# Kernel tuning notes

Measured on AMD Instinct MI355X. Metric: run time of the kernel, lower is better.

Reference implementation:

```python
import jax, jax.numpy as jnp
import numpy as np

B, N, NG, K, H, C, BD = 4, 2048, 12, 16, 64, 128, 64
M = N // 4  # fps with down_sample=4
TWO_PI = 2.0 * np.pi


def _knn_idx(q, x, k):
    # q [Q,3] queries, x [P,3] pool -> [Q,k] indices of k nearest points in x
    d2 = jnp.sum((q[:, None, :] - x[None, :, :]) ** 2, axis=-1)
    _, idx = jax.lax.top_k(-d2, k)
    return idx


def _fps_idx(pos, m):
    # farthest point sampling, fixed m points, start at index 0
    n = pos.shape[0]
    def body(carry, _):
        d, last = carry
        dist = jnp.sum((pos - pos[last]) ** 2, axis=-1)
        d = jnp.minimum(d, dist)
        return (d, jnp.argmax(d)), last
    (_, _), idx = jax.lax.scan(body, (jnp.full((n,), 1e10, pos.dtype), jnp.int32(0)), None, length=m)
    return idx


def _basis_mlp(z, rff_w, w1, b1, w2, b2):
    # RFF -> Linear -> GELU -> Linear -> GELU
    p = TWO_PI * (z @ rff_w)
    f = jnp.concatenate([jnp.sin(p), jnp.cos(p)], axis=-1)
    h = jax.nn.gelu(f @ w1 + b1)
    return jax.nn.gelu(h @ w2 + b2)


def _interaction(x, nbr, kbx, kbR, kx_w, kx_b, kR_w, kR_b, mix_w, mix_b):
    # depthwise separable group conv: spatial gather-multiply-mean, then orientation mix
    kx = kbx @ kx_w + kx_b                     # [M,K,NG,C] spatial depthwise kernel
    kR = kbR @ kR_w + kR_b                     # [NG,NG,C] orientation depthwise kernel
    agg = jnp.mean(x[nbr] * kx, axis=1)        # [M,NG,C] mean over K neighbors
    y = jnp.einsum('bnc,mnc->bmc', agg, kR) / kR.shape[0]
    return x + jax.nn.gelu(y @ mix_w + mix_b)


def setup_inputs():
    key = jax.random.key(0)
    ks = iter(jax.random.split(key, 64))
    def randn(shape, std=1.0):
        return std * jax.random.normal(next(ks), shape, dtype=jnp.float32)
    inp = {}
    inp['pos'] = jax.random.uniform(next(ks), (B, N, 3), dtype=jnp.float32)
    nrm = randn((B, N, 3))
    inp['normal'] = nrm / jnp.linalg.norm(nrm, axis=-1, keepdims=True)
    g = randn((NG, 3))
    inp['grid'] = g / jnp.linalg.norm(g, axis=-1, keepdims=True)
    def lin(name, fin, fout):
        inp[name + '_w'] = randn((fin, fout), 1.0 / np.sqrt(fin))
        inp[name + '_b'] = jnp.zeros((fout,), jnp.float32)
    lin('emb1', 4, H); lin('emb2', H, H)
    lin('down', H, C)
    inp['bx_rff'] = randn((2, C // 2), 10.0)   # sigma=10
    lin('bx1', C, C); lin('bx2', C, BD)
    inp['bR_rff'] = randn((1, C // 2), 10.0)
    lin('bR1', C, C); lin('bR2', C, BD)
    for j in ('i1', 'i2'):
        lin(j + '_kx', BD, C); lin(j + '_kR', BD, C); lin(j + '_mix', C, C)
    lin('post1', C, 256); lin('post2', 256, 64); lin('post3', 64, 1)
    return inp


def reference(pos, normal, grid, emb1_w, emb1_b, emb2_w, emb2_b, down_w, down_b,
              bx_rff, bx1_w, bx1_b, bx2_w, bx2_b, bR_rff, bR1_w, bR1_b, bR2_w, bR2_b,
              i1_kx_w, i1_kx_b, i1_kR_w, i1_kR_b, i1_mix_w, i1_mix_b,
              i2_kx_w, i2_kx_b, i2_kR_w, i2_kR_b, i2_mix_w, i2_mix_b,
              post1_w, post1_b, post2_w, post2_b, post3_w, post3_b):
    def per_graph(p, nm):
        # lift: fiber features = <grid, normal> plus broadcast positions -> [N,NG,4]
        feat = jnp.concatenate([(nm @ grid.T)[:, :, None],
                                jnp.broadcast_to(p[:, None, :], (p.shape[0], NG, 3))], axis=-1)
        x = jax.nn.gelu(feat @ emb1_w + emb1_b) @ emb2_w + emb2_b   # [N,NG,H]
        # downsample block: fps + knn + linear/relu + scatter-max (exactly K edges per target)
        sel = _fps_idx(p, M)
        nbr_d = _knn_idx(p[sel], p, K)                               # [M,K] into N
        h = jax.nn.relu(x @ down_w + down_b)                         # [N,NG,C]
        x = jnp.max(h[nbr_d], axis=1)                                # [M,NG,C]
        ps = p[sel]
        # convolver block: knn graph + r3s2 edge attrs + basis MLPs + 2 interaction layers
        nbr = _knn_idx(ps, ps, K)                                    # [M,K] into M
        rel = ps[nbr] - ps[:, None, :]                               # pos[src]-pos[tgt], [M,K,3]
        rz = jnp.einsum('mke,ne->mkn', rel, grid)                    # [M,K,NG]
        rxy = jnp.sqrt(jnp.sum((rel[:, :, None, :] - rz[..., None] * grid) ** 2, axis=-1) + 1e-12)
        rpx = jnp.stack([rxy, rz], axis=-1)                          # [M,K,NG,2]
        rpR = (grid @ grid.T)[:, :, None]                            # [NG,NG,1]
        kbx = _basis_mlp(rpx, bx_rff, bx1_w, bx1_b, bx2_w, bx2_b)    # [M,K,NG,BD]
        kbR = _basis_mlp(rpR, bR_rff, bR1_w, bR1_b, bR2_w, bR2_b)    # [NG,NG,BD]
        x = _interaction(x, nbr, kbx, kbR, i1_kx_w, i1_kx_b, i1_kR_w, i1_kR_b, i1_mix_w, i1_mix_b)
        x = _interaction(x, nbr, kbx, kbR, i2_kx_w, i2_kx_b, i2_kR_w, i2_kR_b, i2_mix_w, i2_mix_b)
        # readout: mean over grid, global mean pool, MLP head
        g = jnp.mean(x, axis=(0, 1))                                 # [C]
        h1 = jax.nn.gelu(g @ post1_w + post1_b)
        h2 = jax.nn.gelu(h1 @ post2_w + post2_b)
        return h2 @ post3_w + post3_b                                # [1]
    return jax.vmap(per_graph)(pos, normal)                          # [B,1]
```

## Files before the change

### kernel.cpp

```cpp
#include <hip/hip_runtime.h>
#include <hip/hip_bf16.h>
#include <cfloat>

#define B_ 4
#define N_ 2048
#define NG_ 12
#define K_ 16
#define H_ 64
#define C_ 128
#define BD_ 64
#define M_ 512

typedef __attribute__((ext_vector_type(8))) short short8;
typedef __attribute__((ext_vector_type(4))) float floatx4;
typedef unsigned short ushort_t;
typedef unsigned int uint_t;

__device__ __forceinline__ float gelu_f(float x){
  float s = 0.7978845608028654f*(x + 0.044715f*x*x*x);
  float e = __expf(2.0f*s);
  float t = 1.0f - 2.0f/(e + 1.0f);
  return 0.5f*x*(1.0f + t);
}

__device__ __forceinline__ ushort_t bf16_rne(float x){
  uint_t u = __float_as_uint(x);
  uint_t r = (u + 0x7fffu + ((u >> 16) & 1u)) >> 16;
  return (ushort_t)r;
}

__device__ __forceinline__ uint_t pack_hl(float x){
  ushort_t hi = bf16_rne(x);
  float hif = __uint_as_float(((uint_t)hi)<<16);
  ushort_t lo = bf16_rne(x - hif);
  return (uint_t)hi | ((uint_t)lo << 16);
}

__device__ __forceinline__ uint_t cvtpk_bf16(float a, float b){
  uint_t r;
  asm("v_cvt_pk_bf16_f32 %0, %1, %2" : "=v"(r) : "v"(a), "v"(b));
  return r;
}

__device__ __forceinline__ void split2(float v0, float v1, uint_t& hp, uint_t& lp){
  hp = cvtpk_bf16(v0, v1);
  float h0 = __uint_as_float(hp << 16);
  float h1 = __uint_as_float(hp & 0xffff0000u);
  lp = cvtpk_bf16(v0 - h0, v1 - h1);
}

__device__ __forceinline__ uint_t pack_hl2(float v){
  uint_t hp = cvtpk_bf16(v, v);
  float hf = __uint_as_float(hp << 16);
  uint_t lp = cvtpk_bf16(v - hf, v - hf);
  return (hp & 0xffffu) | (lp << 16);
}

__device__ __forceinline__ uint_t perm_lo16(uint_t a, uint_t b){ return __builtin_amdgcn_perm(a, b, 0x05040100u); }
__device__ __forceinline__ uint_t perm_hi16(uint_t a, uint_t b){ return __builtin_amdgcn_perm(a, b, 0x07060302u); }

#define UNPACK8(Q0, Q1, AH, AL) { \
  uint_t* _ap = (uint_t*)&(AH); uint_t* _lp = (uint_t*)&(AL); \
  _ap[0] = perm_lo16((Q0).y, (Q0).x); _ap[1] = perm_lo16((Q0).w, (Q0).z); \
  _ap[2] = perm_lo16((Q1).y, (Q1).x); _ap[3] = perm_lo16((Q1).w, (Q1).z); \
  _lp[0] = perm_hi16((Q0).y, (Q0).x); _lp[1] = perm_hi16((Q0).w, (Q0).z); \
  _lp[2] = perm_hi16((Q1).y, (Q1).x); _lp[3] = perm_hi16((Q1).w, (Q1).z); }

#define DPP_AMAX(CTRL) { \
  int _vb = __float_as_int(v); \
  int _ov = __builtin_amdgcn_update_dpp(_vb, _vb, (CTRL), 0xF, 0xF, false); \
  int _oi = __builtin_amdgcn_update_dpp(vi, vi, (CTRL), 0xF, 0xF, false); \
  float _of = __int_as_float(_ov); \
  bool _tk = (_of > v) || (_of == v && _oi < vi); \
  v = _tk ? _of : v; vi = _tk ? _oi : vi; }

#define DPP_AMIN(CTRL) { \
  int _vb = __float_as_int(v); \
  int _ov = __builtin_amdgcn_update_dpp(_vb, _vb, (CTRL), 0xF, 0xF, false); \
  int _oi = __builtin_amdgcn_update_dpp(vi, vi, (CTRL), 0xF, 0xF, false); \
  float _of = __int_as_float(_ov); \
  bool _tk = (_of < v) || (_of == v && _oi < vi); \
  v = _tk ? _of : v; vi = _tk ? _oi : vi; }

#define FPSB 4
#define LIFTB (B_*N_*NG_/4)
#define WSB 64
#define KBRB (NG_*NG_)
#define PM4B 32

__global__ __launch_bounds__(256) void k_mega1(
    const float* __restrict__ pos, const float* __restrict__ normal,
    const float* __restrict__ grid,
    const float* __restrict__ e1w, const float* __restrict__ e1b,
    const float* __restrict__ e2w, const float* __restrict__ e2b,
    uint_t* __restrict__ x1p, float* __restrict__ ps,
    float4* __restrict__ pos4, float4* __restrict__ ps4,
    const float* __restrict__ bx1w, const float* __restrict__ bx2w,
    const float* __restrict__ kxw1, const float* __restrict__ kxw2,
    const float* __restrict__ dww,
    ushort_t* __restrict__ w1hiT, ushort_t* __restrict__ w1loT,
    ushort_t* __restrict__ w2hiT, ushort_t* __restrict__ w2loT,
    ushort_t* __restrict__ x1hiT, ushort_t* __restrict__ x1loT,
    ushort_t* __restrict__ x2hiT, ushort_t* __restrict__ x2loT,
    ushort_t* __restrict__ dwThi, ushort_t* __restrict__ dwTlo,
    const float* __restrict__ bR_rff,
    const float* __restrict__ bR1w, const float* __restrict__ bR1b,
    const float* __restrict__ bR2w, const float* __restrict__ bR2b,
    const float* __restrict__ kR1w, const float* __restrict__ kR1b,
    const float* __restrict__ kR2w, const float* __restrict__ kR2b,
    float* __restrict__ kRb1, float* __restrict__ kRb2){
  __shared__ float4 posS4[N_];
  __shared__ float2 wred[2][4];
  __shared__ int sidxS[M_];
  __shared__ float ts4[4][64];
  __shared__ float fsb[128], hsb[128];
  int bid = blockIdx.x;
  int tid = threadIdx.x;

  if (bid < FPSB){
    int b = bid;
    for (int i=tid;i<N_;i+=256){
      const float* p = pos + (size_t)b*N_*3 + (size_t)i*3;
      posS4[i] = make_float4(p[0], p[1], p[2], 0.f);
    }
    __syncthreads();
    float px[8],py[8],pz[8],d[8];
    #pragma unroll
    for (int j=0;j<8;++j){
      float4 pt = posS4[tid + 256*j];
      px[j]=pt.x; py[j]=pt.y; pz[j]=pt.z;
      d[j]=1e10f;
    }
    int wave = tid>>6, lane = tid&63;
    int last = 0;
    for (int s=0;s<M_;++s){
      if (tid==0) sidxS[s] = last;
      if (s==M_-1) break;
      float4 lp = posS4[last];
      float lx=lp.x, ly=lp.y, lz=lp.z;
      #pragma unroll
      for (int j=0;j<8;++j){
        float dx=__fsub_rn(px[j],lx), dy=__fsub_rn(py[j],ly), dz=__fsub_rn(pz[j],lz);
        float dist=__fadd_rn(__fadd_rn(__fmul_rn(dx,dx),__fmul_rn(dy,dy)),__fmul_rn(dz,dz));
        d[j]=fminf(d[j],dist);
      }
      float va = d[1]>d[0]?d[1]:d[0]; int ja = d[1]>d[0]?1:0;
      float vb = d[3]>d[2]?d[3]:d[2]; int jb = d[3]>d[2]?3:2;
      float vc = d[5]>d[4]?d[5]:d[4]; int jc = d[5]>d[4]?5:4;
      float vd = d[7]>d[6]?d[7]:d[6]; int jd = d[7]>d[6]?7:6;
      float ve = vb>va?vb:va; int je = vb>va?jb:ja;
      float vf = vd>vc?vd:vc; int jf = vd>vc?jd:jc;
      float v  = vf>ve?vf:ve; int jj = vf>ve?jf:je;
      int vi = tid + (jj<<8);
      DPP_AMAX(0x121); DPP_AMAX(0x122); DPP_AMAX(0x124); DPP_AMAX(0x128);
      DPP_AMAX(0x142); DPP_AMAX(0x143);
      int sv = __builtin_amdgcn_readlane(__float_as_int(v), 63);
      int si = __builtin_amdgcn_readlane(vi, 63);
      if (lane==0) wred[s&1][wave] = make_float2(__int_as_float(sv), __int_as_float(si));
      __syncthreads();
      float2 r0 = wred[s&1][0], r1 = wred[s&1][1], r2 = wred[s&1][2], r3 = wred[s&1][3];
      float bv = r0.x; int bi = __float_as_int(r0.y);
      int i1 = __float_as_int(r1.y); if (r1.x>bv || (r1.x==bv && i1<bi)){ bv=r1.x; bi=i1; }
      int i2 = __float_as_int(r2.y); if (r2.x>bv || (r2.x==bv && i2<bi)){ bv=r2.x; bi=i2; }
      int i3 = __float_as_int(r3.y); if (r3.x>bv || (r3.x==bv && i3<bi)){ bv=r3.x; bi=i3; }
      last = bi;
    }
    __syncthreads();
    for (int i=tid; i<M_; i+=256){
      float4 p = posS4[sidxS[i]];
      float* o = ps + ((size_t)b*M_+i)*3;
      o[0]=p.x; o[1]=p.y; o[2]=p.z;
      ps4[(size_t)b*M_+i] = make_float4(p.x, p.y, p.z, 0.f);
    }
  } else if (bid < FPSB + LIFTB){
    int vbid = bid - FPSB;
    int q = tid>>6, lane = tid&63;
    int fid = vbid*4 + q;
    int g = fid % NG_;
    int n = (fid / NG_) % N_;
    int b = fid / (NG_*N_);
    const float* nm = normal + (size_t)(b*N_+n)*3;
    const float* pp = pos + (size_t)(b*N_+n)*3;
    const float* gg = grid + g*3;
    float f0 = nm[0]*gg[0] + nm[1]*gg[1] + nm[2]*gg[2];
    float t = e1b[lane] + f0*e1w[lane] + pp[0]*e1w[64+lane] + pp[1]*e1w[128+lane] + pp[2]*e1w[192+lane];
    ts4[q][lane] = gelu_f(t);
    __syncthreads();
    float acc = e2b[lane];
    #pragma unroll
    for (int i=0;i<64;++i) acc = fmaf(ts4[q][i], e2w[i*64+lane], acc);
    x1p[(size_t)fid*64 + lane] = pack_hl(acc);
  } else if (bid < FPSB + LIFTB + WSB){
    int tg = (bid - FPSB - LIFTB)*256 + tid;
    if (tg < 16384){
      int j = tg >> 7, k = tg & 127;
      float x = bx1w[k*128 + j];
      ushort_t hi = bf16_rne(x);
      float hif = __uint_as_float(((uint_t)hi)<<16);
      ushort_t lo = bf16_rne(x - hif);
      w1hiT[tg] = hi; w1loT[tg] = lo;
    }
    if (tg < 8192){
      int c = tg >> 7, j = tg & 127;
      float x = bx2w[j*64 + c];
      ushort_t hi = bf16_rne(x);
      float hif = __uint_as_float(((uint_t)hi)<<16);
      ushort_t lo = bf16_rne(x - hif);
      w2hiT[tg] = hi; w2loT[tg] = lo;
    }
    if (tg < 8192){
      int c = tg >> 6, d = tg & 63;
      float xa = kxw1[d*128 + c];
      ushort_t hi = bf16_rne(xa);
      float hif = __uint_as_float(((uint_t)hi)<<16);
      ushort_t lo = bf16_rne(xa - hif);
      x1hiT[tg] = hi; x1loT[tg] = lo;
      float xb = kxw2[d*128 + c];
      ushort_t hi2 = bf16_rne(xb);
      float hif2 = __uint_as_float(((uint_t)hi2)<<16);
      ushort_t lo2 = bf16_rne(xb - hif2);
      x2hiT[tg] = hi2; x2loT[tg] = lo2;
      float xd = dww[d*128 + c];
      ushort_t hi3 = bf16_rne(xd);
      float hif3 = __uint_as_float(((uint_t)hi3)<<16);
      ushort_t lo3 = bf16_rne(xd - hif3);
      dwThi[tg] = hi3; dwTlo[tg] = lo3;
    }
  } else if (bid < FPSB + LIFTB + WSB + KBRB){
    int vbid = bid - FPSB - LIFTB - WSB;
    int gm = vbid / NG_, gn = vbid % NG_;
    int j = tid;
    if (j < 128){
      float z = grid[gm*3]*grid[gn*3] + grid[gm*3+1]*grid[gn*3+1] + grid[gm*3+2]*grid[gn*3+2];
      float ang = 6.283185307179586f * (z * bR_rff[j & 63]);
      fsb[j] = (j<64) ? sinf(ang) : cosf(ang);
    }
    __syncthreads();
    if (j < 128){
      float acc = bR1b[j];
      for (int i=0;i<128;++i) acc = fmaf(fsb[i], bR1w[i*128+j], acc);
      hsb[j] = gelu_f(acc);
    }
    __syncthreads();
    if (j < 64){
      float a2 = bR2b[j];
      for (int i=0;i<128;++i) a2 = fmaf(hsb[i], bR2w[i*64+j], a2);
      fsb[j] = gelu_f(a2);
    }
    __syncthreads();
    if (j < 128){
      float a1 = kR1b[j], a2v = kR2b[j];
      for (int d=0; d<64; ++d){
        float kv = fsb[d];
        a1  = fmaf(kv, kR1w[d*128+j], a1);
        a2v = fmaf(kv, kR2w[d*128+j], a2v);
      }
      kRb1[(size_t)vbid*128 + j] = a1;
      kRb2[(size_t)vbid*128 + j] = a2v;
    }
  } else {
    int i = (bid - FPSB - LIFTB - WSB - KBRB)*256 + tid;
    const float* p = pos + (size_t)i*3;
    pos4[i] = make_float4(p[0], p[1], p[2], 0.f);
  }
}

template<int NP>
__device__ __forceinline__ void knn_body4(int qm, const float4* __restrict__ qp4,
                                          const float4* __restrict__ pool4, int* __restrict__ out){
  constexpr int R = NP/64;
  int lane = threadIdx.x & 63;
  int b = qm / M_;
  float4 q = qp4[qm];
  float qx=q.x, qy=q.y, qz=q.z;
  float d2[R];
  #pragma unroll
  for (int j=0;j<R;++j){
    float4 p = pool4[(size_t)b*NP + lane + 64*j];
    float dx=__fsub_rn(qx,p.x), dy=__fsub_rn(qy,p.y), dz=__fsub_rn(qz,p.z);
    d2[j]=__fadd_rn(__fadd_rn(__fmul_rn(dx,dx),__fmul_rn(dy,dy)),__fmul_rn(dz,dz));
  }
  for (int r=0;r<K_;++r){
    float v=FLT_MAX; int vi=0x7fffffff;
    #pragma unroll
    for (int j=0;j<R;++j){
      if (d2[j]<v){ v=d2[j]; vi=lane+64*j; }
    }
    DPP_AMIN(0x121); DPP_AMIN(0x122); DPP_AMIN(0x124); DPP_AMIN(0x128);
    DPP_AMIN(0x142); DPP_AMIN(0x143);
    int si = __builtin_amdgcn_readlane(vi, 63);
    if (lane==0) out[(size_t)qm*K_ + r] = si;
    #pragma unroll
    for (int j=0;j<R;++j){ if (si == lane + 64*j) d2[j] = FLT_MAX; }
  }
}

__global__ __launch_bounds__(256) void k_knn_all(const float4* __restrict__ ps4,
    const float4* __restrict__ pos4, int* __restrict__ nbrD, int* __restrict__ nbrS){
  int w = threadIdx.x >> 6;
  int bid = blockIdx.x;
  if (bid < B_*M_/4) knn_body4<N_>(bid*4 + w, ps4, pos4, nbrD);
  else               knn_body4<M_>((bid - B_*M_/4)*4 + w, ps4, ps4, nbrS);
}

__device__ __forceinline__ void dm_body(uint_t* um, int bm,
    const uint_t* __restrict__ x1p, const int* __restrict__ nbrD,
    const ushort_t* __restrict__ dwThi, const ushort_t* __restrict__ dwTlo,
    const float* __restrict__ db, float* __restrict__ xA){
  int b = bm / M_;
  int tid = threadIdx.x;
  uint_t* xs = um;
  int* nb = (int*)(um + 12288);
  if (tid < K_) nb[tid] = nbrD[(size_t)bm*K_ + tid];
  __syncthreads();
  for (int idx=tid; idx<3072; idx+=256){
    int k = idx / 192, qq = idx % 192;
    uint4 vv = ((const uint4*)&x1p[((size_t)(b*N_) + nb[k])*(NG_*H_)])[qq];
    int gran = (qq >> 1) ^ (k & 7);
    *(uint4*)&xs[k*768 + gran*8 + (qq&1)*4] = vv;
  }
  __syncthreads();
  int wid = tid>>6, lane = tid&63, ln = lane&15, g4 = lane>>4;
  short8 bh[2][2], bl[2][2];
  float dbv[2];
  #pragma unroll
  for (int nt=0; nt<2; ++nt){
    int col = wid*32 + nt*16 + ln;
    dbv[nt] = db[col];
    #pragma unroll
    for (int ks=0; ks<2; ++ks){
      bh[nt][ks] = *(const short8*)&dwThi[(size_t)col*64 + ks*32 + g4*8];
      bl[nt][ks] = *(const short8*)&dwTlo[(size_t)col*64 + ks*32 + g4*8];
    }
  }
  int xorl = ln & 7;
  #pragma unroll
  for (int g=0; g<NG_; ++g){
    short8 ah[2], al[2];
    #pragma unroll
    for (int ks=0; ks<2; ++ks){
      int col0 = g*64 + ks*32 + g4*8;
      int gran = (col0 >> 3) ^ xorl;
      const uint_t* src = &xs[ln*768 + gran*8];
      uint4 q0 = *(const uint4*)src;
      uint4 q1 = *(const uint4*)(src+4);
      UNPACK8(q0, q1, ah[ks], al[ks]);
    }
    floatx4 acc[2];
    acc[0] = (floatx4){0.f,0.f,0.f,0.f};
    acc[1] = (floatx4){0.f,0.f,0.f,0.f};
    #pragma unroll
    for (int nt=0; nt<2; ++nt)
      #pragma unroll
      for (int ks=0; ks<2; ++ks){
        acc[nt] = __builtin_amdgcn_mfma_f32_16x16x32_bf16(ah[ks], bh[nt][ks], acc[nt], 0,0,0);
        acc[nt] = __builtin_amdgcn_mfma_f32_16x16x32_bf16(al[ks], bh[nt][ks], acc[nt], 0,0,0);
        acc[nt] = __builtin_amdgcn_mfma_f32_16x16x32_bf16(ah[ks], bl[nt][ks], acc[nt], 0,0,0);
      }
    #pragma unroll
    for (int nt=0; nt<2; ++nt){
      float mx = fmaxf(fmaxf(acc[nt][0],acc[nt][1]), fmaxf(acc[nt][2],acc[nt][3]));
      mx = fmaxf(mx, __shfl_xor(mx, 16));
      mx = fmaxf(mx, __shfl_xor(mx, 32));
      if (g4 == 0)
        xA[(size_t)bm*(NG_*C_) + g*C_ + wid*32 + nt*16 + ln] = fmaxf(mx + dbv[nt], 0.0f);
    }
  }
}

__device__ __forceinline__ void kbx_body(float* um, int vbid,
    const float* __restrict__ ps, const int* __restrict__ nbr,
    const float* __restrict__ grid, const float* __restrict__ rff,
    const ushort_t* __restrict__ w1hiT, const ushort_t* __restrict__ w1loT,
    const ushort_t* __restrict__ w2hiT, const ushort_t* __restrict__ w2loT,
    const float* __restrict__ b1, const float* __restrict__ b2,
    uint_t* __restrict__ kbxp){
  float* z0s = um;
  float* z1s = um + 128;
  float* rws = um + 256;
  int tid = threadIdx.x;
  if (tid < 128){
    rws[tid] = rff[tid];
    int fid = vbid*128 + tid;
    int g = fid % NG_;
    int k = (fid/NG_) % K_;
    int bm = fid / (NG_*K_);
    int b = bm / M_;
    int nb = nbr[(size_t)bm*K_ + k];
    const float* pm = ps + (size_t)bm*3;
    const float* pn = ps + ((size_t)(b*M_) + nb)*3;
    float rx = pn[0]-pm[0], ry = pn[1]-pm[1], rz3 = pn[2]-pm[2];
    const float* gg = grid + g*3;
    float rz = rx*gg[0] + ry*gg[1] + rz3*gg[2];
    float vx = rx - rz*gg[0], vy = ry - rz*gg[1], vz = rz3 - rz*gg[2];
    float rxy = sqrtf(vx*vx + vy*vy + vz*vz + 1e-12f);
    z0s[tid]=rxy; z1s[tid]=rz;
  }
  __syncthreads();
  int wid = tid>>6, lane = tid&63;
  int ln = lane & 15, g = lane >> 4;
  float* bw = um + 384 + wid*1088;

  short8 ahi[2][4], alo[2][4];
  #pragma unroll
  for (int rt=0; rt<2; ++rt){
    float z0 = z0s[wid*32 + rt*16 + ln];
    float z1 = z1s[wid*32 + rt*16 + ln];
    #pragma unroll
    for (int ks=0; ks<4; ++ks){
      float vv[8];
      #pragma unroll
      for (int e=0; e<8; ++e){
        int kd = ks*32 + g*8 + e;
        int kk = kd & 63;
        float t = z0*rws[kk] + z1*rws[64+kk];
        t = t - floorf(t);
        vv[e] = (ks < 2) ? __builtin_amdgcn_sinf(t) : __builtin_amdgcn_cosf(t);
      }
      uint_t* hp = (uint_t*)&ahi[rt][ks];
      uint_t* lp = (uint_t*)&alo[rt][ks];
      #pragma unroll
      for (int p=0; p<4; ++p) split2(vv[2*p], vv[2*p+1], hp[p], lp[p]);
    }
  }
  floatx4 acc2[2][4];
  #pragma unroll
  for (int rt=0; rt<2; ++rt)
    #pragma unroll
    for (int ct=0; ct<4; ++ct)
      acc2[rt][ct] = (floatx4){0.f,0.f,0.f,0.f};

  #pragma unroll
  for (int jp=0; jp<4; ++jp){
    floatx4 acc1[2][2];
    #pragma unroll
    for (int rt=0; rt<2; ++rt)
      #pragma unroll
      for (int jt=0; jt<2; ++jt)
        acc1[rt][jt] = (floatx4){0.f,0.f,0.f,0.f};
    #pragma unroll
    for (int ks=0; ks<4; ++ks){
      #pragma unroll
      for (int jt=0; jt<2; ++jt){
        int j = jp*32 + jt*16 + ln;
        short8 bhi = *(const short8*)&w1hiT[(size_t)j*128 + ks*32 + g*8];
        short8 blo = *(const short8*)&w1loT[(size_t)j*128 + ks*32 + g*8];
        #pragma unroll
        for (int rt=0; rt<2; ++rt){
          acc1[rt][jt] = __builtin_amdgcn_mfma_f32_16x16x32_bf16(ahi[rt][ks], bhi, acc1[rt][jt], 0,0,0);
          acc1[rt][jt] = __builtin_amdgcn_mfma_f32_16x16x32_bf16(alo[rt][ks], bhi, acc1[rt][jt], 0,0,0);
          acc1[rt][jt] = __builtin_amdgcn_mfma_f32_16x16x32_bf16(ahi[rt][ks], blo, acc1[rt][jt], 0,0,0);
        }
      }
    }
    #pragma unroll
    for (int jt=0; jt<2; ++jt){
      float bb = b1[jp*32 + jt*16 + ln];
      #pragma unroll
      for (int rt=0; rt<2; ++rt)
        #pragma unroll
        for (int i=0; i<4; ++i)
          bw[(rt*16 + g*4 + i)*34 + jt*16 + ln] = gelu_f(bb + acc1[rt][jt][i]);
    }
    #pragma unroll
    for (int rt=0; rt<2; ++rt){
      int base = (rt*16 + ln)*34 + g*8;
      float2 p0 = *(float2*)&bw[base+0];
      float2 p1 = *(float2*)&bw[base+2];
      float2 p2 = *(float2*)&bw[base+4];
      float2 p3 = *(float2*)&bw[base+6];
      short8 a2h, a2l;
      uint_t* hp = (uint_t*)&a2h;
      uint_t* lp = (uint_t*)&a2l;
      split2(p0.x, p0.y, hp[0], lp[0]);
      split2(p1.x, p1.y, hp[1], lp[1]);
      split2(p2.x, p2.y, hp[2], lp[2]);
      split2(p3.x, p3.y, hp[3], lp[3]);
      #pragma unroll
      for (int ct=0; ct<4; ++ct){
        short8 b2h = *(const short8*)&w2hiT[(size_t)(ct*16+ln)*128 + jp*32 + g*8];
        short8 b2l = *(const short8*)&w2loT[(size_t)(ct*16+ln)*128 + jp*32 + g*8];
        acc2[rt][ct] = __builtin_amdgcn_mfma_f32_16x16x32_bf16(a2h, b2h, acc2[rt][ct], 0,0,0);
        acc2[rt][ct] = __builtin_amdgcn_mfma_f32_16x16x32_bf16(a2l, b2h, acc2[rt][ct], 0,0,0);
        acc2[rt][ct] = __builtin_amdgcn_mfma_f32_16x16x32_bf16(a2h, b2l, acc2[rt][ct], 0,0,0);
      }
    }
  }
  #pragma unroll
  for (int ct=0; ct<4; ++ct){
    float bb = b2[ct*16 + ln];
    #pragma unroll
    for (int rt=0; rt<2; ++rt)
      #pragma unroll
      for (int i=0; i<4; ++i){
        int row = wid*32 + rt*16 + g*4 + i;
        size_t fiber = (size_t)vbid*128 + row;
        kbxp[fiber*64 + ct*16 + ln] = pack_hl2(gelu_f(bb + acc2[rt][ct][i]));
      }
  }
}

__global__ __launch_bounds__(256) void k_dmkbx(
    const uint_t* __restrict__ x1p, const int* __restrict__ nbrD,
    const ushort_t* __restrict__ dwThi, const ushort_t* __restrict__ dwTlo,
    const float* __restrict__ db, float* __restrict__ xA,
    const float* __restrict__ ps, const int* __restrict__ nbrS,
    const float* __restrict__ grid, const float* __restrict__ rff,
    const ushort_t* __restrict__ w1hiT, const ushort_t* __restrict__ w1loT,
    const ushort_t* __restrict__ w2hiT, const ushort_t* __restrict__ w2loT,
    const float* __restrict__ b1, const float* __restrict__ b2,
    uint_t* __restrict__ kbxp){
  __shared__ __align__(16) uint_t um[12384];
  int bid = blockIdx.x;
  if (bid < B_*M_)
    dm_body(um, bid, x1p, nbrD, dwThi, dwTlo, db, xA);
  else
    kbx_body((float*)um, bid - B_*M_, ps, nbrS, grid, rff, w1hiT, w1loT, w2hiT, w2loT, b1, b2, kbxp);
}

__global__ __launch_bounds__(256) void k_inter(
    const float* __restrict__ xin, const int* __restrict__ nbr,
    const uint_t* __restrict__ kbxp, const float* __restrict__ kR,
    const ushort_t* __restrict__ kxhT, const ushort_t* __restrict__ kxlT,
    const float* __restrict__ kxb,
    const float* __restrict__ mw, const float* __restrict__ mb,
    float* __restrict__ xout, float* __restrict__ part){
  int bm = blockIdx.x; int b = bm / M_;
  int tid = threadIdx.x;
  int wid = tid>>6, lane = tid&63, ln = lane&15, g4 = lane>>4;
  int c = tid & 127, gh = tid >> 7;
  __shared__ uint_t kbsL[48][68];
  __shared__ __align__(16) float TsU[48*129];
  float* aggS_ = TsU;
  float* yS_   = TsU + 1536;
  float* psumS_= TsU + 3072;

  const uint4* ksrc = (const uint4*)(kbxp + (size_t)bm*192*64);

  uint4 ka = ksrc[tid], kbv = ksrc[tid+256], kc = ksrc[tid+512];
  int nb0 = nbr[(size_t)bm*K_+0], nb1 = nbr[(size_t)bm*K_+1],
      nb2 = nbr[(size_t)bm*K_+2], nb3 = nbr[(size_t)bm*K_+3];

  short8 bh[2][2], bl[2][2];
  float kxbv[2];
  #pragma unroll
  for (int nt=0; nt<2; ++nt){
    int cc_ = (wid*2+nt)*16 + ln;
    kxbv[nt] = kxb[cc_];
    #pragma unroll
    for (int ks=0; ks<2; ++ks){
      bh[nt][ks] = *(const short8*)&kxhT[(size_t)cc_*64 + ks*32 + g4*8];
      bl[nt][ks] = *(const short8*)&kxlT[(size_t)cc_*64 + ks*32 + g4*8];
    }
  }
  float accg[6] = {0,0,0,0,0,0};

  for (int cc=0; cc<4; ++cc){
    {
      int i0=tid, i1=tid+256, i2=tid+512;
      *(uint4*)&kbsL[i0>>4][(i0&15)*4] = ka;
      *(uint4*)&kbsL[i1>>4][(i1&15)*4] = kbv;
      *(uint4*)&kbsL[i2>>4][(i2&15)*4] = kc;
    }
    __syncthreads();
    float xreg[24];
    {
      const float* xr0 = xin + ((size_t)(b*M_) + nb0)*(NG_*C_);
      const float* xr1 = xin + ((size_t)(b*M_) + nb1)*(NG_*C_);
      const float* xr2 = xin + ((size_t)(b*M_) + nb2)*(NG_*C_);
      const float* xr3 = xin + ((size_t)(b*M_) + nb3)*(NG_*C_);
      #pragma unroll
      for (int gi=0; gi<6; ++gi){
        int off = (gh*6+gi)*C_ + c;
        xreg[0*6+gi] = xr0[off];
        xreg[1*6+gi] = xr1[off];
        xreg[2*6+gi] = xr2[off];
        xreg[3*6+gi] = xr3[off];
      }
    }
    if (cc < 3){
      ka  = ksrc[(cc+1)*768 + tid];
      kbv = ksrc[(cc+1)*768 + tid + 256];
      kc  = ksrc[(cc+1)*768 + tid + 512];
      nb0 = nbr[(size_t)bm*K_ + (cc+1)*4 + 0];
      nb1 = nbr[(size_t)bm*K_ + (cc+1)*4 + 1];
      nb2 = nbr[(size_t)bm*K_ + (cc+1)*4 + 2];
      nb3 = nbr[(size_t)bm*K_ + (cc+1)*4 + 3];
    }
    floatx4 acc[3][2];
    #pragma unroll
    for (int mt=0; mt<3; ++mt)
      #pragma unroll
      for (int nt=0; nt<2; ++nt)
        acc[mt][nt] = (floatx4){0.f,0.f,0.f,0.f};
    #pragma unroll
    for (int mt=0; mt<3; ++mt){
      short8 ah[2], al[2];
      #pragma unroll
      for (int ks=0; ks<2; ++ks){
        const uint_t* src = &kbsL[mt*16+ln][ks*32+g4*8];
        uint4 q0 = *(const uint4*)src;
        uint4 q1 = *(const uint4*)(src+4);
        UNPACK8(q0, q1, ah[ks], al[ks]);
      }
      #pragma unroll
      for (int nt=0; nt<2; ++nt)
        #pragma unroll
        for (int ks=0; ks<2; ++ks){
          acc[mt][nt] = __builtin_amdgcn_mfma_f32_16x16x32_bf16(ah[ks], bh[nt][ks], acc[mt][nt], 0,0,0);
          acc[mt][nt] = __builtin_amdgcn_mfma_f32_16x16x32_bf16(al[ks], bh[nt][ks], acc[mt][nt], 0,0,0);
          acc[mt][nt] = __builtin_amdgcn_mfma_f32_16x16x32_bf16(ah[ks], bl[nt][ks], acc[mt][nt], 0,0,0);
        }
    }
    #pragma unroll
    for (int mt=0; mt<3; ++mt)
      #pragma unroll
      for (int nt=0; nt<2; ++nt)
        #pragma unroll
        for (int i=0; i<4; ++i)
          TsU[(mt*16 + g4*4 + i)*129 + (wid*2+nt)*16 + ln] = acc[mt][nt][i] + kxbv[nt];
    __syncthreads();
    #pragma unroll
    for (int kl=0; kl<4; ++kl)
      #pragma unroll
      for (int gi=0; gi<6; ++gi)
        accg[gi] = fmaf(TsU[(kl*12 + gh*6 + gi)*129 + c], xreg[kl*6+gi], accg[gi]);
    __syncthreads();
  }
  #pragma unroll
  for (int gi=0; gi<6; ++gi)
    aggS_[(gh*6+gi)*C_ + c] = accg[gi] * (1.0f/16.0f);
  __syncthreads();
  #pragma unroll
  for (int gi=0; gi<6; ++gi){
    int g = gh*6+gi;
    float yv = 0.f;
    #pragma unroll
    for (int n=0;n<NG_;++n) yv = fmaf(aggS_[n*C_ + c], kR[((size_t)g*NG_+n)*C_ + c], yv);
    yS_[g*C_ + c] = yv * (1.0f/12.0f);
  }
  __syncthreads();
  float m6[6] = {0,0,0,0,0,0};
  for (int i4=0;i4<32;++i4){
    float w0 = mw[(i4*4+0)*C_+c], w1 = mw[(i4*4+1)*C_+c],
          w2 = mw[(i4*4+2)*C_+c], w3 = mw[(i4*4+3)*C_+c];
    #pragma unroll
    for (int gi=0;gi<6;++gi){
      int g = gh*6+gi;
      float4 yv = *(const float4*)&yS_[g*C_ + i4*4];
      m6[gi] = fmaf(yv.x,w0,fmaf(yv.y,w1,fmaf(yv.z,w2,fmaf(yv.w,w3,m6[gi]))));
    }
  }
  float mbc = mb[c];
  float psum = 0.f;
  #pragma unroll
  for (int gi=0;gi<6;++gi){
    int g = gh*6+gi;
    size_t off = (size_t)bm*(NG_*C_) + g*C_ + c;
    float val = xin[off] + gelu_f(m6[gi] + mbc);
    xout[off] = val;
    psum += val;
  }
  if (part){
    psumS_[gh*C_ + c] = psum;
    __syncthreads();
    if (gh == 0)
      part[(size_t)bm*C_ + c] = psumS_[c] + psumS_[C_ + c];
  }
}

__global__ __launch_bounds__(256) void k_head(
    const float* __restrict__ part,
    const float* __restrict__ p1w, const float* __restrict__ p1b,
    const float* __restrict__ p2w, const float* __restrict__ p2b,
    const float* __restrict__ p3w, const float* __restrict__ p3b,
    float* __restrict__ out){
  int b = blockIdx.x, tid = threadIdx.x;
  int c = tid & 127, half = tid >> 7;
  __shared__ float red[256];
  __shared__ float gs[128];
  {
    const float* pb = part + (size_t)b*M_*C_;
    float a0=0.f,a1=0.f,a2=0.f,a3=0.f;
    for (int r = half*4; r < M_; r += 8){
      a0 += pb[(size_t)(r+0)*C_ + c];
      a1 += pb[(size_t)(r+1)*C_ + c];
      a2 += pb[(size_t)(r+2)*C_ + c];
      a3 += pb[(size_t)(r+3)*C_ + c];
    }
    red[tid] = (a0+a1)+(a2+a3);
  }
  __syncthreads();
  if (half==0) gs[c] = (red[c] + red[128+c]) * (1.0f/(M_*NG_));
  __syncthreads();
  __shared__ float h1[256];
  {
    float a = p1b[tid];
    for (int i=0;i<128;++i) a = fmaf(gs[i], p1w[i*256+tid], a);
    h1[tid] = gelu_f(a);
  }
  __syncthreads();
  __shared__ float h2[64];
  if (tid<64){
    float a = p2b[tid];
    for (int i=0;i<256;++i) a = fmaf(h1[i], p2w[i*64+tid], a);
    h2[tid] = gelu_f(a);
  }
  __syncthreads();
  if (tid==0){
    float a = p3b[0];
    for (int i=0;i<64;++i) a = fmaf(h2[i], p3w[i], a);
    out[b] = a;
  }
}

extern "C" void kernel_launch(void* const* d_in, const int* in_sizes, int n_in,
                              void* d_out, int out_size, void* d_ws, size_t ws_size,
                              hipStream_t stream){
  const float* pos    = (const float*)d_in[0];
  const float* normal = (const float*)d_in[1];
  const float* grid   = (const float*)d_in[2];
  const float* e1w = (const float*)d_in[3];  const float* e1b = (const float*)d_in[4];
  const float* e2w = (const float*)d_in[5];  const float* e2b = (const float*)d_in[6];
  const float* dww = (const float*)d_in[7];  const float* dwb = (const float*)d_in[8];
  const float* bx_rff = (const float*)d_in[9];
  const float* bx1w = (const float*)d_in[10]; const float* bx1b = (const float*)d_in[11];
  const float* bx2w = (const float*)d_in[12]; const float* bx2b = (const float*)d_in[13];
  const float* bR_rff = (const float*)d_in[14];
  const float* bR1w = (const float*)d_in[15]; const float* bR1b = (const float*)d_in[16];
  const float* bR2w = (const float*)d_in[17]; const float* bR2b = (const float*)d_in[18];
  const float* i1kxw = (const float*)d_in[19]; const float* i1kxb = (const float*)d_in[20];
  const float* i1kRw = (const float*)d_in[21]; const float* i1kRb = (const float*)d_in[22];
  const float* i1mw  = (const float*)d_in[23]; const float* i1mb  = (const float*)d_in[24];
  const float* i2kxw = (const float*)d_in[25]; const float* i2kxb = (const float*)d_in[26];
  const float* i2kRw = (const float*)d_in[27]; const float* i2kRb = (const float*)d_in[28];
  const float* i2mw  = (const float*)d_in[29]; const float* i2mb  = (const float*)d_in[30];
  const float* p1w = (const float*)d_in[31]; const float* p1b = (const float*)d_in[32];
  const float* p2w = (const float*)d_in[33]; const float* p2b = (const float*)d_in[34];
  const float* p3w = (const float*)d_in[35]; const float* p3b = (const float*)d_in[36];
  float* out = (float*)d_out;

  float* ws = (float*)d_ws;
  size_t o = 0;
  uint_t* x1p = (uint_t*)(ws + o); o += (size_t)B_*N_*NG_*H_;
  float* psb = ws + o; o += (size_t)B_*M_*3;
  float* xA  = ws + o; o += (size_t)B_*M_*NG_*C_;
  float* xB  = ws + o; o += (size_t)B_*M_*NG_*C_;
  uint_t* kbxp = (uint_t*)(ws + o); o += (size_t)B_*M_*K_*NG_*BD_;
  float* kRb1 = ws + o; o += (size_t)NG_*NG_*C_;
  float* kRb2 = ws + o; o += (size_t)NG_*NG_*C_;
  float* part = ws + o; o += (size_t)B_*M_*C_;
  float4* pos4 = (float4*)(ws + o); o += (size_t)B_*N_*4;
  float4* ps4  = (float4*)(ws + o); o += (size_t)B_*M_*4;
  int* nbrD  = (int*)(ws + o); o += (size_t)B_*M_*K_;
  int* nbrS  = (int*)(ws + o); o += (size_t)B_*M_*K_;
  ushort_t* w1hiT = (ushort_t*)(ws + o); o += 8192;
  ushort_t* w1loT = (ushort_t*)(ws + o); o += 8192;
  ushort_t* w2hiT = (ushort_t*)(ws + o); o += 4096;
  ushort_t* w2loT = (ushort_t*)(ws + o); o += 4096;
  ushort_t* x1hiT = (ushort_t*)(ws + o); o += 4096;
  ushort_t* x1loT = (ushort_t*)(ws + o); o += 4096;
  ushort_t* x2hiT = (ushort_t*)(ws + o); o += 4096;
  ushort_t* x2loT = (ushort_t*)(ws + o); o += 4096;
  ushort_t* dwThi = (ushort_t*)(ws + o); o += 4096;
  ushort_t* dwTlo = (ushort_t*)(ws + o); o += 4096;

  k_mega1<<<FPSB + LIFTB + WSB + KBRB + PM4B, 256, 0, stream>>>(
      pos, normal, grid, e1w, e1b, e2w, e2b, x1p, psb, pos4, ps4,
      bx1w, bx2w, i1kxw, i2kxw, dww,
      w1hiT, w1loT, w2hiT, w2loT, x1hiT, x1loT, x2hiT, x2loT, dwThi, dwTlo,
      bR_rff, bR1w, bR1b, bR2w, bR2b,
      i1kRw, i1kRb, i2kRw, i2kRb, kRb1, kRb2);
  k_knn_all<<<B_*M_/2, 256, 0, stream>>>(ps4, pos4, nbrD, nbrS);
  k_dmkbx<<<B_*M_ + (B_*M_*K_*NG_)/128, 256, 0, stream>>>(
      x1p, nbrD, dwThi, dwTlo, dwb, xA,
      psb, nbrS, grid, bx_rff, w1hiT, w1loT, w2hiT, w2loT, bx1b, bx2b, kbxp);
  k_inter<<<B_*M_, 256, 0, stream>>>(xA, nbrS, kbxp, kRb1, x1hiT, x1loT, i1kxb, i1mw, i1mb, xB, nullptr);
  k_inter<<<B_*M_, 256, 0, stream>>>(xB, nbrS, kbxp, kRb2, x2hiT, x2loT, i2kxb, i2mw, i2mb, xA, part);
  k_head<<<B_, 256, 0, stream>>>(part, p1w, p1b, p2w, p2b, p3w, p3b, out);
}
```

Before: 732.6 us.

## Precompute dense kNN for all points in parallel with FPS, then look up

Instead of running the down-sampling kNN (FPS centers vs full cloud) after farthest point sampling, the first fused kernel now computes 16-NN for every one of the N points per batch in extra blocks that run alongside the serial FPS blocks. FPS writes out its selected indices, and the down-sample stage looks up neighbor lists by sampled index. This takes the dense kNN off the critical path behind FPS, at the cost of doing 4x more kNN queries than needed and reading pos without float4 packing.

```diff
diff --git a/kernel.cpp b/kernel.cpp
--- a/kernel.cpp
+++ b/kernel.cpp
@@ -87,6 +87,7 @@
 #define WSB 64
 #define KBRB (NG_*NG_)
 #define PM4B 32
+#define AKB (B_*N_/4)
 
 __global__ __launch_bounds__(256) void k_mega1(
     const float* __restrict__ pos, const float* __restrict__ normal,
@@ -95,6 +96,7 @@
     const float* __restrict__ e2w, const float* __restrict__ e2b,
     uint_t* __restrict__ x1p, float* __restrict__ ps,
     float4* __restrict__ pos4, float4* __restrict__ ps4,
+    int* __restrict__ sidxG, int* __restrict__ allD,
     const float* __restrict__ bx1w, const float* __restrict__ bx2w,
     const float* __restrict__ kxw1, const float* __restrict__ kxw2,
     const float* __restrict__ dww,
@@ -167,10 +169,12 @@
     }
     __syncthreads();
     for (int i=tid; i<M_; i+=256){
-      float4 p = posS4[sidxS[i]];
+      int si = sidxS[i];
+      float4 p = posS4[si];
       float* o = ps + ((size_t)b*M_+i)*3;
       o[0]=p.x; o[1]=p.y; o[2]=p.z;
       ps4[(size_t)b*M_+i] = make_float4(p.x, p.y, p.z, 0.f);
+      sidxG[(size_t)b*M_+i] = si;
     }
   } else if (bid < FPSB + LIFTB){
     int vbid = bid - FPSB;
@@ -258,10 +262,36 @@
       kRb1[(size_t)vbid*128 + j] = a1;
       kRb2[(size_t)vbid*128 + j] = a2v;
     }
-  } else {
+  } else if (bid < FPSB + LIFTB + WSB + KBRB + PM4B){
     int i = (bid - FPSB - LIFTB - WSB - KBRB)*256 + tid;
     const float* p = pos + (size_t)i*3;
     pos4[i] = make_float4(p[0], p[1], p[2], 0.f);
+  } else {
+    int w = tid>>6, lane = tid&63;
+    int qi = (bid - FPSB - LIFTB - WSB - KBRB - PM4B)*4 + w;
+    int b = qi / N_;
+    const float* q = pos + (size_t)qi*3;
+    float qx=q[0], qy=q[1], qz=q[2];
+    float d2[32];
+    #pragma unroll
+    for (int j=0;j<32;++j){
+      const float* p = pos + ((size_t)(b*N_) + lane + 64*j)*3;
+      float dx=__fsub_rn(qx,p[0]), dy=__fsub_rn(qy,p[1]), dz=__fsub_rn(qz,p[2]);
+      d2[j]=__fadd_rn(__fadd_rn(__fmul_rn(dx,dx),__fmul_rn(dy,dy)),__fmul_rn(dz,dz));
+    }
+    for (int r=0;r<K_;++r){
+      float v=FLT_MAX; int vi=0x7fffffff;
+      #pragma unroll
+      for (int j=0;j<32;++j){
+        if (d2[j]<v){ v=d2[j]; vi=lane+64*j; }
+      }
+      DPP_AMIN(0x121); DPP_AMIN(0x122); DPP_AMIN(0x124); DPP_AMIN(0x128);
+      DPP_AMIN(0x142); DPP_AMIN(0x143);
+      int si = __builtin_amdgcn_readlane(vi, 63);
+      if (lane==0) allD[(size_t)qi*K_ + r] = si;
+      #pragma unroll
+      for (int j=0;j<32;++j){ if (si == lane + 64*j) d2[j] = FLT_MAX; }
+    }
   }
 }
 
@@ -296,22 +326,21 @@
 }
 
 __global__ __launch_bounds__(256) void k_knn_all(const float4* __restrict__ ps4,
-    const float4* __restrict__ pos4, int* __restrict__ nbrD, int* __restrict__ nbrS){
+    int* __restrict__ nbrS){
   int w = threadIdx.x >> 6;
-  int bid = blockIdx.x;
-  if (bid < B_*M_/4) knn_body4<N_>(bid*4 + w, ps4, pos4, nbrD);
-  else               knn_body4<M_>((bid - B_*M_/4)*4 + w, ps4, ps4, nbrS);
+  knn_body4<M_>(blockIdx.x*4 + w, ps4, ps4, nbrS);
 }
 
 __device__ __forceinline__ void dm_body(uint_t* um, int bm,
-    const uint_t* __restrict__ x1p, const int* __restrict__ nbrD,
+    const uint_t* __restrict__ x1p,
+    const int* __restrict__ sidxG, const int* __restrict__ allD,
     const ushort_t* __restrict__ dwThi, const ushort_t* __restrict__ dwTlo,
     const float* __restrict__ db, float* __restrict__ xA){
   int b = bm / M_;
   int tid = threadIdx.x;
   uint_t* xs = um;
   int* nb = (int*)(um + 12288);
-  if (tid < K_) nb[tid] = nbrD[(size_t)bm*K_ + tid];
+  if (tid < K_) nb[tid] = allD[((size_t)(b*N_) + sidxG[bm])*K_ + tid];
   __syncthreads();
   for (int idx=tid; idx<3072; idx+=256){
     int k = idx / 192, qq = idx % 192;
@@ -501,7 +530,8 @@
 }
 
 __global__ __launch_bounds__(256) void k_dmkbx(
-    const uint_t* __restrict__ x1p, const int* __restrict__ nbrD,
+    const uint_t* __restrict__ x1p,
+    const int* __restrict__ sidxG, const int* __restrict__ allD,
     const ushort_t* __restrict__ dwThi, const ushort_t* __restrict__ dwTlo,
     const float* __restrict__ db, float* __restrict__ xA,
     const float* __restrict__ ps, const int* __restrict__ nbrS,
@@ -513,7 +543,7 @@
   __shared__ __align__(16) uint_t um[12384];
   int bid = blockIdx.x;
   if (bid < B_*M_)
-    dm_body(um, bid, x1p, nbrD, dwThi, dwTlo, db, xA);
+    dm_body(um, bid, x1p, sidxG, allD, dwThi, dwTlo, db, xA);
   else
     kbx_body((float*)um, bid - B_*M_, ps, nbrS, grid, rff, w1hiT, w1loT, w2hiT, w2loT, b1, b2, kbxp);
 }
@@ -752,7 +782,8 @@
   float* part = ws + o; o += (size_t)B_*M_*C_;
   float4* pos4 = (float4*)(ws + o); o += (size_t)B_*N_*4;
   float4* ps4  = (float4*)(ws + o); o += (size_t)B_*M_*4;
-  int* nbrD  = (int*)(ws + o); o += (size_t)B_*M_*K_;
+  int* sidxG = (int*)(ws + o); o += (size_t)B_*M_;
+  int* allD  = (int*)(ws + o); o += (size_t)B_*N_*K_;
   int* nbrS  = (int*)(ws + o); o += (size_t)B_*M_*K_;
   ushort_t* w1hiT = (ushort_t*)(ws + o); o += 8192;
   ushort_t* w1loT = (ushort_t*)(ws + o); o += 8192;
@@ -765,15 +796,15 @@
   ushort_t* dwThi = (ushort_t*)(ws + o); o += 4096;
   ushort_t* dwTlo = (ushort_t*)(ws + o); o += 4096;
 
-  k_mega1<<<FPSB + LIFTB + WSB + KBRB + PM4B, 256, 0, stream>>>(
-      pos, normal, grid, e1w, e1b, e2w, e2b, x1p, psb, pos4, ps4,
+  k_mega1<<<FPSB + LIFTB + WSB + KBRB + PM4B + AKB, 256, 0, stream>>>(
+      pos, normal, grid, e1w, e1b, e2w, e2b, x1p, psb, pos4, ps4, sidxG, allD,
       bx1w, bx2w, i1kxw, i2kxw, dww,
       w1hiT, w1loT, w2hiT, w2loT, x1hiT, x1loT, x2hiT, x2loT, dwThi, dwTlo,
       bR_rff, bR1w, bR1b, bR2w, bR2b,
       i1kRw, i1kRb, i2kRw, i2kRb, kRb1, kRb2);
-  k_knn_all<<<B_*M_/2, 256, 0, stream>>>(ps4, pos4, nbrD, nbrS);
+  k_knn_all<<<B_*M_/4, 256, 0, stream>>>(ps4, nbrS);
   k_dmkbx<<<B_*M_ + (B_*M_*K_*NG_)/128, 256, 0, stream>>>(
-      x1p, nbrD, dwThi, dwTlo, dwb, xA,
+      x1p, sidxG, allD, dwThi, dwTlo, dwb, xA,
       psb, nbrS, grid, bx_rff, w1hiT, w1loT, w2hiT, w2loT, bx1b, bx2b, kbxp);
   k_inter<<<B_*M_, 256, 0, stream>>>(xA, nbrS, kbxp, kRb1, x1hiT, x1loT, i1kxb, i1mw, i1mb, xB, nullptr);
   k_inter<<<B_*M_, 256, 0, stream>>>(xB, nbrS, kbxp, kRb2, x2hiT, x2loT, i2kxb, i2mw, i2mb, xA, part);
```

Measured after the change: 722.7 us. No clear change (-1.4%).
